# Kernel tuning notes

Measured on AMD Instinct MI355X. Metric: run time of the kernel, lower is better.

Reference implementation:

```python
import jax, jax.numpy as jnp
import numpy as np

B, N, F_IN, F_OUT, E, GSD = 64, 512, 512, 512, 4, 1024
EPS = 1e-5


def _bn(z2d, gamma, beta):
    # training-mode BatchNorm1d over rows, biased variance, eps=1e-5
    mean = z2d.mean(axis=0)
    var = z2d.var(axis=0)
    return (z2d - mean) * jax.lax.rsqrt(var + EPS) * gamma + beta


def setup_inputs() -> dict:
    key = jax.random.key(0)
    ks = jax.random.split(key, 10)
    x = jax.random.normal(ks[0], (B, N, F_IN), dtype=jnp.float32)
    adj = jax.random.uniform(ks[1], (B, E, N, N), dtype=jnp.float32)
    global_state = jax.random.normal(ks[2], (B, GSD), dtype=jnp.float32)
    subgraph_sizes = jax.random.randint(ks[3], (B, 2), 0, 256, dtype=jnp.int64)
    mask = jnp.ones((B, N, 1), dtype=jnp.float32)
    # parameters
    W_gfc = jax.random.normal(ks[4], (GSD // 2, F_OUT), dtype=jnp.float32) * (1.0 / np.sqrt(GSD // 2))
    b_gfc = jnp.zeros((F_OUT,), dtype=jnp.float32)
    W_gc = jax.random.normal(ks[5], (E, F_IN + F_OUT, F_OUT), dtype=jnp.float32) * (1.0 / np.sqrt(F_IN + F_OUT))
    b_gc = jnp.zeros((F_OUT,), dtype=jnp.float32)
    gamma_n = jnp.ones((F_OUT,), dtype=jnp.float32)
    beta_n = jnp.zeros((F_OUT,), dtype=jnp.float32)
    gamma_g = jnp.ones((F_OUT,), dtype=jnp.float32)
    beta_g = jnp.zeros((F_OUT,), dtype=jnp.float32)
    return dict(x=x, adj=adj, global_state=global_state, subgraph_sizes=subgraph_sizes,
                mask=mask, W_gfc=W_gfc, b_gfc=b_gfc, W_gc=W_gc, b_gc=b_gc,
                gamma_n=gamma_n, beta_n=beta_n, gamma_g=gamma_g, beta_g=beta_g)


def reference(x, adj, global_state, subgraph_sizes, mask,
              W_gfc, b_gfc, W_gc, b_gc, gamma_n, beta_n, gamma_g, beta_g):
    b, n, _ = x.shape
    o = W_gfc.shape[1]
    # global FC on the two halves of the global state
    gs = global_state.reshape(b, 2, -1)                 # [B,2,GSD/2]
    gt = jnp.einsum('bkg,go->bko', gs, W_gfc) + b_gfc   # [B,2,O]
    # data-dependent broadcast of global features into node slices (vectorized)
    n1 = subgraph_sizes[:, 0]
    n2 = subgraph_sizes[:, 1]
    idx = jnp.arange(n)[None, :]
    sel0 = (idx < n1[:, None]).astype(x.dtype)                                  # [B,N]
    sel1 = ((idx >= n1[:, None]) & (idx < (n1 + n2)[:, None])).astype(x.dtype)  # [B,N]
    bg = sel0[..., None] * gt[:, 0, None, :] + sel1[..., None] * gt[:, 1, None, :]  # [B,N,O]
    x_concat = jnp.concatenate([x, bg], axis=-1)        # [B,N,F_IN+O]
    # multi-relational graph convolution: sum_e adj_e @ (x W_e) + bias
    support = jnp.einsum('bnf,efo->beno', x_concat, W_gc)       # [B,E,N,O]
    x_out = jnp.einsum('benm,bemo->bno', adj, support) + b_gc   # [B,N,O]
    # BN + mask + relu on nodes
    x_out = _bn(x_out.reshape(-1, o), gamma_n, beta_n).reshape(b, n, o)
    x_out = jax.nn.relu(x_out * mask)
    # BN + relu on global
    g_out = _bn(gt.reshape(-1, o), gamma_g, beta_g).reshape(b, 2, o)
    g_out = jax.nn.relu(g_out).reshape(b, -1)
    return x_out, g_out
```

## Files before the change

kernel.cpp:

```cpp
#include <hip/hip_runtime.h>

#define DEVI __device__ __forceinline__

typedef __bf16 bf16x8 __attribute__((ext_vector_type(8)));
typedef float  f32x4  __attribute__((ext_vector_type(4)));
typedef unsigned short ushort8_t __attribute__((ext_vector_type(8)));

constexpr size_t XOUT_ELEMS = (size_t)64 * 512 * 512;

DEVI unsigned short f2b(float f) {
  __bf16 h = (__bf16)f;
  return __builtin_bit_cast(unsigned short, h);
}

__global__ void k_decode(const int* __restrict__ ss, int* __restrict__ ns) {
  int t = threadIdx.x;
  int odd = ss[2 * t + 1];
  unsigned long long bal = __ballot(odd == 0);
  bool is64 = (bal == 0xFFFFFFFFFFFFFFFFull);
  if (is64) {
    const long long* s64 = (const long long*)ss;
    ns[2 * t]     = (int)s64[2 * t];
    ns[2 * t + 1] = (int)s64[2 * t + 1];
  } else {
    ns[2 * t]     = ss[2 * t];
    ns[2 * t + 1] = ss[2 * t + 1];
  }
}

__global__ void k_gt(const float* __restrict__ gs, const float* __restrict__ W,
                     const float* __restrict__ bias, float* __restrict__ gt,
                     unsigned short* __restrict__ gth) {
  __shared__ float srow[4][512];
  int r0  = blockIdx.y * 4;
  int col = blockIdx.x * 256 + threadIdx.x;
  for (int i = threadIdx.x; i < 4 * 512; i += 256)
    srow[i >> 9][i & 511] = gs[(size_t)r0 * 512 + i];
  __syncthreads();
  float acc[4] = {0.f, 0.f, 0.f, 0.f};
  for (int g = 0; g < 512; ++g) {
    float w = W[(size_t)g * 512 + col];
    acc[0] += srow[0][g] * w;
    acc[1] += srow[1][g] * w;
    acc[2] += srow[2][g] * w;
    acc[3] += srow[3][g] * w;
  }
  float bb = bias[col];
  #pragma unroll
  for (int r = 0; r < 4; ++r) {
    float v = acc[r] + bb;
    gt [(size_t)(r0 + r) * 512 + col] = v;
    gth[(size_t)(r0 + r) * 512 + col] = f2b(v);
  }
}

__global__ void k_gbn(const float* __restrict__ gt, const float* __restrict__ gamma,
                      const float* __restrict__ beta, float* __restrict__ gout) {
  int col = blockIdx.x * 64 + threadIdx.x;
  float s = 0.f, q = 0.f;
  for (int r = 0; r < 128; ++r) {
    float v = gt[(size_t)r * 512 + col];
    s += v; q += v * v;
  }
  float m   = s * (1.f / 128.f);
  float var = q * (1.f / 128.f) - m * m;
  float inv = 1.f / sqrtf(var + 1e-5f);
  float g = gamma[col], b = beta[col];
  for (int r = 0; r < 128; ++r) {
    float v = (gt[(size_t)r * 512 + col] - m) * inv * g + b;
    gout[(size_t)r * 512 + col] = fmaxf(v, 0.f);
  }
}

__global__ void k_cvt(const float* __restrict__ in, unsigned short* __restrict__ out,
                      long n8) {
  long i = (long)blockIdx.x * blockDim.x + threadIdx.x;
  long stride = (long)gridDim.x * blockDim.x;
  for (; i < n8; i += stride) {
    float4 a = ((const float4*)in)[2 * i];
    float4 b = ((const float4*)in)[2 * i + 1];
    ushort8_t o;
    o[0] = f2b(a.x); o[1] = f2b(a.y); o[2] = f2b(a.z); o[3] = f2b(a.w);
    o[4] = f2b(b.x); o[5] = f2b(b.y); o[6] = f2b(b.z); o[7] = f2b(b.w);
    *(ushort8_t*)&out[i * 8] = o;
  }
}

__global__ void k_cvt_w(const float* __restrict__ W, unsigned short* __restrict__ wT) {
  __shared__ float t[32][33];
  int k0 = blockIdx.x * 32, o0 = blockIdx.y * 32, e = blockIdx.z;
  const float* Wb = W + (size_t)e * 1024 * 512;
  unsigned short* Tb = wT + (size_t)e * 512 * 1024;
  int tid = threadIdx.x;
  #pragma unroll
  for (int p = 0; p < 4; ++p) {
    int kl = p * 8 + (tid >> 5), ol = tid & 31;
    t[kl][ol] = Wb[(size_t)(k0 + kl) * 512 + o0 + ol];
  }
  __syncthreads();
  #pragma unroll
  for (int p = 0; p < 4; ++p) {
    int ol = p * 8 + (tid >> 5), kl = tid & 31;
    Tb[(size_t)(o0 + ol) * 1024 + k0 + kl] = f2b(t[kl][ol]);
  }
}

DEVI void gl_lds16(const unsigned short* g, unsigned short* l) {
  __builtin_amdgcn_global_load_lds(
      (const __attribute__((address_space(1))) void*)g,
      (__attribute__((address_space(3))) void*)l, 16, 0, 0);
}

DEVI int lds_idx(int row, int slot) {
  return row * 32 + ((slot ^ ((row >> 1) & 3)) << 3);
}

template <class FA, class FB>
DEVI void mfma_core(unsigned short* As, unsigned short* Bs, FA srcA, FB srcB,
                    int NT, f32x4 (&acc)[4][4]) {
  const int tid  = threadIdx.x;
  const int lane = tid & 63;
  const int wave = tid >> 6;
  const int wr = wave >> 1, wc = wave & 1;
  const int fr = lane & 15, fs = lane >> 4;

  const int c0 = tid,       r0 = c0 >> 2, s0 = (c0 & 3) ^ ((r0 >> 1) & 3);
  const int c1 = tid + 256, r1 = c1 >> 2, s1 = (c1 & 3) ^ ((r1 >> 1) & 3);

  int aoff[4], boff[4];
  #pragma unroll
  for (int i = 0; i < 4; ++i) {
    aoff[i] = lds_idx(wr * 64 + i * 16 + fr, fs);
    boff[i] = lds_idx(wc * 64 + i * 16 + fr, fs);
  }

  gl_lds16(srcA(r0, s0 * 8, 0), As + c0 * 8);
  gl_lds16(srcA(r1, s1 * 8, 0), As + c1 * 8);
  gl_lds16(srcB(r0, s0 * 8, 0), Bs + c0 * 8);
  gl_lds16(srcB(r1, s1 * 8, 0), Bs + c1 * 8);

  for (int kt = 0; kt < NT; ++kt) {
    __syncthreads();
    bf16x8 af[4], bfv[4];
    #pragma unroll
    for (int i = 0; i < 4; ++i) af[i] = *(const bf16x8*)(As + aoff[i]);
    #pragma unroll
    for (int j = 0; j < 4; ++j) bfv[j] = *(const bf16x8*)(Bs + boff[j]);
    if (kt + 1 < NT) {
      __syncthreads();
      gl_lds16(srcA(r0, s0 * 8, kt + 1), As + c0 * 8);
      gl_lds16(srcA(r1, s1 * 8, kt + 1), As + c1 * 8);
      gl_lds16(srcB(r0, s0 * 8, kt + 1), Bs + c0 * 8);
      gl_lds16(srcB(r1, s1 * 8, kt + 1), Bs + c1 * 8);
    }
    #pragma unroll
    for (int i = 0; i < 4; ++i)
      #pragma unroll
      for (int j = 0; j < 4; ++j)
        acc[i][j] = __builtin_amdgcn_mfma_f32_16x16x32_bf16(af[i], bfv[j], acc[i][j], 0, 0, 0);
  }
}

__global__ __launch_bounds__(256) void k_gadd(
    const unsigned short* __restrict__ gth, const unsigned short* __restrict__ wT,
    float* __restrict__ gadd) {
  __shared__ __align__(16) unsigned short As[4096], Bs[4096];
  const int otile = blockIdx.x * 128;

  auto srcA = [=](int row, int kofs, int kt) -> const unsigned short* {
    return gth + (size_t)row * 512 + kt * 32 + kofs;
  };
  auto srcB = [=](int row, int kofs, int kt) -> const unsigned short* {
    int op = otile + row;
    int e = op >> 9, o = op & 511;
    return wT + (size_t)e * 524288 + (size_t)o * 1024 + 512 + kt * 32 + kofs;
  };

  f32x4 acc[4][4];
  #pragma unroll
  for (int i = 0; i < 4; ++i)
    #pragma unroll
    for (int j = 0; j < 4; ++j) acc[i][j] = (f32x4){0.f, 0.f, 0.f, 0.f};

  mfma_core(As, Bs, srcA, srcB, 16, acc);

  const int lane = threadIdx.x & 63, wave = threadIdx.x >> 6;
  const int wr = wave >> 1, wc = wave & 1, fr = lane & 15, fs = lane >> 4;
  #pragma unroll
  for (int i = 0; i < 4; ++i) {
    int m = wr * 64 + i * 16 + fs * 4;
    #pragma unroll
    for (int j = 0; j < 4; ++j) {
      int op = otile + wc * 64 + j * 16 + fr;
      #pragma unroll
      for (int r = 0; r < 4; ++r)
        gadd[(size_t)(m + r) * 2048 + op] = acc[i][j][r];
    }
  }
}

template <class FA, class FB>
DEVI void core256(unsigned short* lds, FA srcA, FB srcB, int NT, f32x4 (&acc)[8][4]) {
  const int tid  = threadIdx.x;
  const int lane = tid & 63;
  const int wave = tid >> 6;
  const int wr = wave >> 2, wcol = wave & 3;
  const int fr = lane & 15, fs = lane >> 4;

  int crow[2], cslot[2];
  #pragma unroll
  for (int t = 0; t < 2; ++t) {
    int c = tid + t * 512;
    crow[t]  = c >> 2;
    cslot[t] = (c & 3) ^ ((crow[t] >> 1) & 3);
  }

  int aoff[8], boff[4];
  #pragma unroll
  for (int i = 0; i < 8; ++i) {
    int row = wr * 128 + i * 16 + fr;
    aoff[i] = row * 32 + ((fs ^ ((row >> 1) & 3)) << 3);
  }
  #pragma unroll
  for (int j = 0; j < 4; ++j) {
    int row = wcol * 64 + j * 16 + fr;
    boff[j] = row * 32 + ((fs ^ ((row >> 1) & 3)) << 3);
  }

  #pragma unroll
  for (int t = 0; t < 2; ++t) {
    int c = tid + t * 512;
    gl_lds16(srcA(crow[t], cslot[t] * 8, 0), lds + c * 8);
    gl_lds16(srcB(crow[t], cslot[t] * 8, 0), lds + 8192 + c * 8);
  }
  __syncthreads();

  int cur = 0;
  for (int kt = 0; kt < NT; ++kt) {
    unsigned short* Ab = lds + (cur ? 16384 : 0);
    unsigned short* Bb = Ab + 8192;
    if (kt + 1 < NT) {
      unsigned short* An = lds + (cur ? 0 : 16384);
      unsigned short* Bn = An + 8192;
      #pragma unroll
      for (int t = 0; t < 2; ++t) {
        int c = tid + t * 512;
        gl_lds16(srcA(crow[t], cslot[t] * 8, kt + 1), An + c * 8);
        gl_lds16(srcB(crow[t], cslot[t] * 8, kt + 1), Bn + c * 8);
      }
    }
    bf16x8 af[8], bfv[4];
    #pragma unroll
    for (int i = 0; i < 8; ++i) af[i] = *(const bf16x8*)(Ab + aoff[i]);
    #pragma unroll
    for (int j = 0; j < 4; ++j) bfv[j] = *(const bf16x8*)(Bb + boff[j]);
    #pragma unroll
    for (int i = 0; i < 8; ++i)
      #pragma unroll
      for (int j = 0; j < 4; ++j)
        acc[i][j] = __builtin_amdgcn_mfma_f32_16x16x32_bf16(af[i], bfv[j], acc[i][j], 0, 0, 0);
    __syncthreads();
    cur ^= 1;
  }
}

__global__ __launch_bounds__(512) void k_support(
    const unsigned short* __restrict__ xh, const unsigned short* __restrict__ wT,
    const float* __restrict__ gadd, const int* __restrict__ ns,
    unsigned short* __restrict__ supT) {
  __shared__ __align__(16) unsigned short lds[32768];
  const int xcd = blockIdx.x & 7;
  const int jj  = blockIdx.x >> 3;
  const int et  = jj & 15;
  const int e    = et >> 2;
  const int tile = et & 3;
  const int zi  = (jj >> 4) * 8 + xcd;
  const int row0  = (tile >> 1) * 256;
  const int otile = (tile & 1) * 256;
  const int b = zi;
  const int n1  = ns[2 * b];
  const int n12 = n1 + ns[2 * b + 1];
  const unsigned short* xb = xh + (size_t)b * 262144;
  const unsigned short* wb = wT + (size_t)e * 524288;

  auto srcA = [=](int r, int koff, int kt) -> const unsigned short* {
    return xb + (size_t)(row0 + r) * 512 + kt * 32 + koff;
  };
  auto srcB = [=](int r, int koff, int kt) -> const unsigned short* {
    return wb + (size_t)(otile + r) * 1024 + kt * 32 + koff;
  };

  f32x4 acc[8][4];
  #pragma unroll
  for (int i = 0; i < 8; ++i)
    #pragma unroll
    for (int j = 0; j < 4; ++j) acc[i][j] = (f32x4){0.f, 0.f, 0.f, 0.f};

  core256(lds, srcA, srcB, 16, acc);

  const int lane = threadIdx.x & 63, wave = threadIdx.x >> 6;
  const int wr = wave >> 2, wcol = wave & 3, fr = lane & 15, fs = lane >> 4;
  unsigned short* sp = supT + (size_t)(zi * 4 + e) * 262144;
  #pragma unroll
  for (int j = 0; j < 4; ++j) {
    int o = otile + wcol * 64 + j * 16 + fr;
    float g0 = gadd[(size_t)(2 * b)     * 2048 + e * 512 + o];
    float g1 = gadd[(size_t)(2 * b + 1) * 2048 + e * 512 + o];
    #pragma unroll
    for (int i = 0; i < 8; ++i) {
      int m = row0 + wr * 128 + i * 16 + fs * 4;
      ushort4 h;
      #pragma unroll
      for (int r = 0; r < 4; ++r) {
        int mr = m + r;
        float add = (mr < n1) ? g0 : ((mr < n12) ? g1 : 0.f);
        ((unsigned short*)&h)[r] = f2b(acc[i][j][r] + add);
      }
      *(ushort4*)&sp[(size_t)o * 512 + m] = h;
    }
  }
}

__global__ __launch_bounds__(512) void k_xout(
    const unsigned short* __restrict__ adjh, const unsigned short* __restrict__ supT,
    const float* __restrict__ bgc, float* __restrict__ out,
    float* __restrict__ gsum, float* __restrict__ gsq) {
  __shared__ __align__(16) unsigned short lds[32768];
  const int xcd = blockIdx.x & 7;
  const int jj  = blockIdx.x >> 3;
  const int tile = jj & 3;
  const int zi  = (jj >> 2) * 8 + xcd;
  const int row0  = (tile >> 1) * 256;
  const int otile = (tile & 1) * 256;
  const int b = zi;
  const unsigned short* ab = adjh + (size_t)b * 4 * 262144;
  const unsigned short* sb = supT + (size_t)zi * 4 * 262144;

  auto srcA = [=](int r, int koff, int kt) -> const unsigned short* {
    int k = kt * 32 + koff;
    int e = k >> 9, m = k & 511;
    return ab + ((size_t)e * 512 + row0 + r) * 512 + m;
  };
  auto srcB = [=](int r, int koff, int kt) -> const unsigned short* {
    int k = kt * 32 + koff;
    int e = k >> 9, m = k & 511;
    return sb + (size_t)e * 262144 + (size_t)(otile + r) * 512 + m;
  };

  f32x4 acc[8][4];
  #pragma unroll
  for (int i = 0; i < 8; ++i)
    #pragma unroll
    for (int j = 0; j < 4; ++j) acc[i][j] = (f32x4){0.f, 0.f, 0.f, 0.f};

  core256(lds, srcA, srcB, 64, acc);

  const int tid = threadIdx.x;
  const int lane = tid & 63, wave = tid >> 6;
  const int wr = wave >> 2, wcol = wave & 3, fr = lane & 15, fs = lane >> 4;

  float cs[4], cq[4];
  #pragma unroll
  for (int j = 0; j < 4; ++j) {
    int o = otile + wcol * 64 + j * 16 + fr;
    float bb = bgc[o];
    float s = 0.f, q = 0.f;
    #pragma unroll
    for (int i = 0; i < 8; ++i) {
      int nb = row0 + wr * 128 + i * 16 + fs * 4;
      #pragma unroll
      for (int r = 0; r < 4; ++r) {
        float v = acc[i][j][r] + bb;
        out[((size_t)b * 512 + nb + r) * 512 + o] = v;
        s += v; q += v * v;
      }
    }
    cs[j] = s; cq[j] = q;
  }

  float* red = (float*)lds;
  __syncthreads();
  red[tid] = 0.f;
  __syncthreads();
  #pragma unroll
  for (int j = 0; j < 4; ++j) {
    int cl = wcol * 64 + j * 16 + fr;
    atomicAdd(&red[cl], cs[j]);
    atomicAdd(&red[256 + cl], cq[j]);
  }
  __syncthreads();
  if (tid < 256) {
    atomicAdd(&gsum[otile + tid], red[tid]);
    atomicAdd(&gsq[otile + tid],  red[256 + tid]);
  }
}

__global__ void k_norm(const float* __restrict__ gsum, const float* __restrict__ gsq,
                       const float* __restrict__ gamma, const float* __restrict__ beta,
                       const float* __restrict__ mask, float* __restrict__ out) {
  __shared__ float sc[512], sh[512];
  for (int c = threadIdx.x; c < 512; c += blockDim.x) {
    float m   = gsum[c] * (1.f / 32768.f);
    float var = gsq[c] * (1.f / 32768.f) - m * m;
    float inv = 1.f / sqrtf(var + 1e-5f);
    float g = gamma[c] * inv;
    sc[c] = g;
    sh[c] = beta[c] - m * g;
  }
  __syncthreads();
  size_t i0 = (size_t)blockIdx.x * blockDim.x + threadIdx.x;
  size_t stride = (size_t)gridDim.x * blockDim.x;
  size_t n4 = XOUT_ELEMS / 4;
  for (size_t i = i0; i < n4; i += stride) {
    float4 p = ((const float4*)out)[i];
    int c = (int)((i * 4) & 511);
    size_t row = (i * 4) >> 9;
    float mk = mask[row];
    p.x = fmaxf((p.x * sc[c + 0] + sh[c + 0]) * mk, 0.f);
    p.y = fmaxf((p.y * sc[c + 1] + sh[c + 1]) * mk, 0.f);
    p.z = fmaxf((p.z * sc[c + 2] + sh[c + 2]) * mk, 0.f);
    p.w = fmaxf((p.w * sc[c + 3] + sh[c + 3]) * mk, 0.f);
    ((float4*)out)[i] = p;
  }
}

extern "C" void kernel_launch(void* const* d_in, const int* in_sizes, int n_in,
                              void* d_out, int out_size, void* d_ws, size_t ws_size,
                              hipStream_t stream) {
  const float* x    = (const float*)d_in[0];
  const float* adj  = (const float*)d_in[1];
  const float* gs   = (const float*)d_in[2];
  const int*   ssz  = (const int*)d_in[3];
  const float* mask = (const float*)d_in[4];
  const float* Wgfc = (const float*)d_in[5];
  const float* bgfc = (const float*)d_in[6];
  const float* Wgc  = (const float*)d_in[7];
  const float* bgc  = (const float*)d_in[8];
  const float* gn   = (const float*)d_in[9];
  const float* btn  = (const float*)d_in[10];
  const float* gg   = (const float*)d_in[11];
  const float* btg  = (const float*)d_in[12];
  float* out = (float*)d_out;

  char* w = (char*)d_ws;
  float*          gt   = (float*)w;
  unsigned short* gth  = (unsigned short*)(w + 262144);
  float*          gadd = (float*)(w + 393216);
  int*            ns   = (int*)(w + 1441792);
  float*          gsum = (float*)(w + 1442304);
  float*          gsq  = (float*)(w + 1444352);
  unsigned short* xh   = (unsigned short*)(w + ((size_t)2  << 20));
  unsigned short* wT   = (unsigned short*)(w + ((size_t)34 << 20));
  unsigned short* adjh = (unsigned short*)(w + ((size_t)40 << 20));
  unsigned short* supT = (unsigned short*)(w + ((size_t)168 << 20));

  k_decode<<<1, 64, 0, stream>>>(ssz, ns);
  k_gt<<<dim3(2, 32), 256, 0, stream>>>(gs, Wgfc, bgfc, gt, gth);
  k_gbn<<<8, 64, 0, stream>>>(gt, gg, btg, out + XOUT_ELEMS);
  hipMemsetAsync(gsum, 0, 4096, stream);

  k_cvt<<<2048, 256, 0, stream>>>(x, xh, (long)(16777216 / 8));
  k_cvt<<<4096, 256, 0, stream>>>(adj, adjh, (long)(67108864 / 8));
  k_cvt_w<<<dim3(32, 16, 4), 256, 0, stream>>>(Wgc, wT);
  k_gadd<<<16, 256, 0, stream>>>(gth, wT, gadd);

  k_support<<<1024, 512, 0, stream>>>(xh, wT, gadd, ns, supT);
  k_xout<<<256, 512, 0, stream>>>(adjh, supT, bgc, out, gsum, gsq);

  k_norm<<<2048, 256, 0, stream>>>(gsum, gsq, gn, btn, mask, out);
}
```

Baseline: 745.2 us.

## Fuse fp32-to-bf16 conversion of x and adj into GEMM operand loads

Removes the separate conversion passes for x and adj. The GEMM kernels now read fp32 A tiles from global memory into registers, convert them to bf16 after the MFMA block, and store them into swizzled LDS. This cuts the full write and re-read of the bf16 copies, about 384MB of traffic for adj. In exchange, A loads go through registers instead of direct global-to-LDS copies, which adds register pressure and moves conversion ALU work inside the MFMA loop. The k_support kernel now re-reads x in fp32 from every block that uses it.

```diff
diff --git a/kernel.cpp b/kernel.cpp
--- a/kernel.cpp
+++ b/kernel.cpp
@@ -72,20 +72,6 @@
   }
 }
 
-__global__ void k_cvt(const float* __restrict__ in, unsigned short* __restrict__ out,
-                      long n8) {
-  long i = (long)blockIdx.x * blockDim.x + threadIdx.x;
-  long stride = (long)gridDim.x * blockDim.x;
-  for (; i < n8; i += stride) {
-    float4 a = ((const float4*)in)[2 * i];
-    float4 b = ((const float4*)in)[2 * i + 1];
-    ushort8_t o;
-    o[0] = f2b(a.x); o[1] = f2b(a.y); o[2] = f2b(a.z); o[3] = f2b(a.w);
-    o[4] = f2b(b.x); o[5] = f2b(b.y); o[6] = f2b(b.z); o[7] = f2b(b.w);
-    *(ushort8_t*)&out[i * 8] = o;
-  }
-}
-
 __global__ void k_cvt_w(const float* __restrict__ W, unsigned short* __restrict__ wT) {
   __shared__ float t[32][33];
   int k0 = blockIdx.x * 32, o0 = blockIdx.y * 32, e = blockIdx.z;
@@ -207,12 +193,20 @@
   const int wr = wave >> 2, wcol = wave & 3;
   const int fr = lane & 15, fs = lane >> 4;
 
-  int crow[2], cslot[2];
+  int arow[2], aslot[2], aidx[2];
   #pragma unroll
   for (int t = 0; t < 2; ++t) {
     int c = tid + t * 512;
-    crow[t]  = c >> 2;
-    cslot[t] = (c & 3) ^ ((crow[t] >> 1) & 3);
+    arow[t] = c >> 2;
+    aslot[t] = c & 3;
+    aidx[t] = arow[t] * 32 + ((aslot[t] ^ ((arow[t] >> 1) & 3)) << 3);
+  }
+  int brow[2], bslot[2];
+  #pragma unroll
+  for (int t = 0; t < 2; ++t) {
+    int c = tid + t * 512;
+    brow[t]  = c >> 2;
+    bslot[t] = (c & 3) ^ ((brow[t] >> 1) & 3);
   }
 
   int aoff[8], boff[4];
@@ -229,9 +223,18 @@
 
   #pragma unroll
   for (int t = 0; t < 2; ++t) {
+    const float* p = srcA(arow[t], aslot[t] * 8, 0);
+    float4 v0 = *(const float4*)p;
+    float4 v1 = *(const float4*)(p + 4);
+    ushort8_t h;
+    h[0] = f2b(v0.x); h[1] = f2b(v0.y); h[2] = f2b(v0.z); h[3] = f2b(v0.w);
+    h[4] = f2b(v1.x); h[5] = f2b(v1.y); h[6] = f2b(v1.z); h[7] = f2b(v1.w);
+    *(ushort8_t*)(lds + aidx[t]) = h;
+  }
+  #pragma unroll
+  for (int t = 0; t < 2; ++t) {
     int c = tid + t * 512;
-    gl_lds16(srcA(crow[t], cslot[t] * 8, 0), lds + c * 8);
-    gl_lds16(srcB(crow[t], cslot[t] * 8, 0), lds + 8192 + c * 8);
+    gl_lds16(srcB(brow[t], bslot[t] * 8, 0), lds + 8192 + c * 8);
   }
   __syncthreads();
 
@@ -239,14 +242,18 @@
   for (int kt = 0; kt < NT; ++kt) {
     unsigned short* Ab = lds + (cur ? 16384 : 0);
     unsigned short* Bb = Ab + 8192;
-    if (kt + 1 < NT) {
-      unsigned short* An = lds + (cur ? 0 : 16384);
-      unsigned short* Bn = An + 8192;
+    const bool more = (kt + 1 < NT);
+    float4 fa0_0, fa0_1, fa1_0, fa1_1;
+    if (more) {
+      const float* p0 = srcA(arow[0], aslot[0] * 8, kt + 1);
+      const float* p1 = srcA(arow[1], aslot[1] * 8, kt + 1);
+      fa0_0 = *(const float4*)p0; fa0_1 = *(const float4*)(p0 + 4);
+      fa1_0 = *(const float4*)p1; fa1_1 = *(const float4*)(p1 + 4);
+      unsigned short* Bn = lds + (cur ? 0 : 16384) + 8192;
       #pragma unroll
       for (int t = 0; t < 2; ++t) {
         int c = tid + t * 512;
-        gl_lds16(srcA(crow[t], cslot[t] * 8, kt + 1), An + c * 8);
-        gl_lds16(srcB(crow[t], cslot[t] * 8, kt + 1), Bn + c * 8);
+        gl_lds16(srcB(brow[t], bslot[t] * 8, kt + 1), Bn + c * 8);
       }
     }
     bf16x8 af[8], bfv[4];
@@ -259,13 +266,23 @@
       #pragma unroll
       for (int j = 0; j < 4; ++j)
         acc[i][j] = __builtin_amdgcn_mfma_f32_16x16x32_bf16(af[i], bfv[j], acc[i][j], 0, 0, 0);
+    if (more) {
+      unsigned short* An = lds + (cur ? 0 : 16384);
+      ushort8_t h0, h1;
+      h0[0] = f2b(fa0_0.x); h0[1] = f2b(fa0_0.y); h0[2] = f2b(fa0_0.z); h0[3] = f2b(fa0_0.w);
+      h0[4] = f2b(fa0_1.x); h0[5] = f2b(fa0_1.y); h0[6] = f2b(fa0_1.z); h0[7] = f2b(fa0_1.w);
+      h1[0] = f2b(fa1_0.x); h1[1] = f2b(fa1_0.y); h1[2] = f2b(fa1_0.z); h1[3] = f2b(fa1_0.w);
+      h1[4] = f2b(fa1_1.x); h1[5] = f2b(fa1_1.y); h1[6] = f2b(fa1_1.z); h1[7] = f2b(fa1_1.w);
+      *(ushort8_t*)(An + aidx[0]) = h0;
+      *(ushort8_t*)(An + aidx[1]) = h1;
+    }
     __syncthreads();
     cur ^= 1;
   }
 }
 
 __global__ __launch_bounds__(512) void k_support(
-    const unsigned short* __restrict__ xh, const unsigned short* __restrict__ wT,
+    const float* __restrict__ x, const unsigned short* __restrict__ wT,
     const float* __restrict__ gadd, const int* __restrict__ ns,
     unsigned short* __restrict__ supT) {
   __shared__ __align__(16) unsigned short lds[32768];
@@ -280,10 +297,10 @@
   const int b = zi;
   const int n1  = ns[2 * b];
   const int n12 = n1 + ns[2 * b + 1];
-  const unsigned short* xb = xh + (size_t)b * 262144;
+  const float* xb = x + (size_t)b * 262144;
   const unsigned short* wb = wT + (size_t)e * 524288;
 
-  auto srcA = [=](int r, int koff, int kt) -> const unsigned short* {
+  auto srcA = [=](int r, int koff, int kt) -> const float* {
     return xb + (size_t)(row0 + r) * 512 + kt * 32 + koff;
   };
   auto srcB = [=](int r, int koff, int kt) -> const unsigned short* {
@@ -322,7 +339,7 @@
 }
 
 __global__ __launch_bounds__(512) void k_xout(
-    const unsigned short* __restrict__ adjh, const unsigned short* __restrict__ supT,
+    const float* __restrict__ adj, const unsigned short* __restrict__ supT,
     const float* __restrict__ bgc, float* __restrict__ out,
     float* __restrict__ gsum, float* __restrict__ gsq) {
   __shared__ __align__(16) unsigned short lds[32768];
@@ -333,10 +350,10 @@
   const int row0  = (tile >> 1) * 256;
   const int otile = (tile & 1) * 256;
   const int b = zi;
-  const unsigned short* ab = adjh + (size_t)b * 4 * 262144;
+  const float* ab = adj + (size_t)b * 1048576;
   const unsigned short* sb = supT + (size_t)zi * 4 * 262144;
 
-  auto srcA = [=](int r, int koff, int kt) -> const unsigned short* {
+  auto srcA = [=](int r, int koff, int kt) -> const float* {
     int k = kt * 32 + koff;
     int e = k >> 9, m = k & 511;
     return ab + ((size_t)e * 512 + row0 + r) * 512 + m;
@@ -449,9 +466,7 @@
   int*            ns   = (int*)(w + 1441792);
   float*          gsum = (float*)(w + 1442304);
   float*          gsq  = (float*)(w + 1444352);
-  unsigned short* xh   = (unsigned short*)(w + ((size_t)2  << 20));
   unsigned short* wT   = (unsigned short*)(w + ((size_t)34 << 20));
-  unsigned short* adjh = (unsigned short*)(w + ((size_t)40 << 20));
   unsigned short* supT = (unsigned short*)(w + ((size_t)168 << 20));
 
   k_decode<<<1, 64, 0, stream>>>(ssz, ns);
@@ -459,13 +474,11 @@
   k_gbn<<<8, 64, 0, stream>>>(gt, gg, btg, out + XOUT_ELEMS);
   hipMemsetAsync(gsum, 0, 4096, stream);
 
-  k_cvt<<<2048, 256, 0, stream>>>(x, xh, (long)(16777216 / 8));
-  k_cvt<<<4096, 256, 0, stream>>>(adj, adjh, (long)(67108864 / 8));
   k_cvt_w<<<dim3(32, 16, 4), 256, 0, stream>>>(Wgc, wT);
   k_gadd<<<16, 256, 0, stream>>>(gth, wT, gadd);
 
-  k_support<<<1024, 512, 0, stream>>>(xh, wT, gadd, ns, supT);
-  k_xout<<<256, 512, 0, stream>>>(adjh, supT, bgc, out, gsum, gsq);
+  k_support<<<1024, 512, 0, stream>>>(x, wT, gadd, ns, supT);
+  k_xout<<<256, 512, 0, stream>>>(adj, supT, bgc, out, gsum, gsq);
 
   k_norm<<<2048, 256, 0, stream>>>(gsum, gsq, gn, btn, mask, out);
 }
```

Result: faster. 719.6 us (-3.4%).
